# Optimization experiments

Hardware: AMD Instinct MI355X
Metric: run time of the kernel (lower is better)

Reference implementation:

```python
import jax, jax.numpy as jnp
import numpy as np

SQ, B, NH, HD = 2048, 2, 16, 128  # seq, batch, heads, head_dim


def setup_inputs() -> dict:
    key = jax.random.key(0)
    kq, kk, kv = jax.random.split(key, 3)
    shape = (SQ, B, NH, HD)
    return {
        "query": jax.random.normal(kq, shape, dtype=jnp.float32),
        "key": jax.random.normal(kk, shape, dtype=jnp.float32),
        "value": jax.random.normal(kv, shape, dtype=jnp.float32),
        "attention_mask": jnp.ones((B, 1, SQ, SQ), dtype=bool),
    }


def reference(query, key, value, attention_mask):
    # query/key/value: [s, b, n, h]
    sq, b, n_heads, hn = query.shape
    norm_factor = jnp.sqrt(jnp.asarray(hn, query.dtype))
    # QK^T -> [b, n, sq, sk]
    scores = jnp.einsum("sbnh,tbnh->bnst", query, key) / norm_factor
    probs = jax.nn.softmax(scores, axis=-1, where=attention_mask)
    # PV -> [s, b, n, h]  (dropout is identity at p=0.0 / eval)
    context = jnp.einsum("bnst,tbnh->sbnh", probs, value)
    return context.reshape(sq, b, n_heads * hn)
```

## Files before the change

### kernel.cpp

```cpp
#include <hip/hip_runtime.h>
#include <hip/hip_bf16.h>
#include <math.h>


#define SQ 2048
#define NBH 32
#define HD 128
#define RSTRIDE 4096
#define BQ 256
#define BK 64
#define NKT (SQ / BK)
#define HELEMS (SQ * HD)
#define SCALE_LOG2E 0.12751879523499918f
#define THR_LOG2 8.0f

typedef __attribute__((ext_vector_type(4)))  float f32x4;
typedef __attribute__((ext_vector_type(16))) float f32x16;
typedef __attribute__((ext_vector_type(4)))  short s16x4;
typedef __attribute__((ext_vector_type(8)))  short s16x8;

#define MFMA32(a, b, c) __builtin_amdgcn_mfma_f32_32x32x16_bf16((a), (b), (c), 0, 0, 0)
#define WAITV(N) asm volatile("s_waitcnt vmcnt(" #N ")" ::: "memory")

__device__ __forceinline__ short f2bf(float f) {
    __hip_bfloat16 h = __float2bfloat16(f);
    return __builtin_bit_cast(short, h);
}
__device__ __forceinline__ unsigned pk2(float lo, float hi) {
    unsigned r;
    asm("v_cvt_pk_bf16_f32 %0, %1, %2" : "=v"(r) : "v"(lo), "v"(hi));
    return r;
}

__device__ __forceinline__ void stage16(const void* g, void* l) {
    __builtin_amdgcn_global_load_lds(
        (const __attribute__((address_space(1))) unsigned int*)g,
        (__attribute__((address_space(3))) unsigned int*)l, 16, 0, 0);
}

__global__ __launch_bounds__(256) void prep_qk(const float* __restrict__ Q,
                                               const float* __restrict__ K,
                                               short* __restrict__ wq,
                                               short* __restrict__ wk) {
    const int id = blockIdx.x * 256 + threadIdx.x;
    const int bh = id >> 15;
    const int s  = (id >> 4) & 2047;
    const int c  = id & 15;
    const size_t outoff = (size_t)bh * HELEMS + (size_t)s * HD + c * 8;
    {
        const float* src = Q + (size_t)s * RSTRIDE + bh * HD + c * 8;
        f32x4 a = *(const f32x4*)src;
        f32x4 b = *(const f32x4*)(src + 4);
        s16x8 f;
        #pragma unroll
        for (int j = 0; j < 4; ++j) {
            f[j]     = f2bf(a[j] * SCALE_LOG2E);
            f[4 + j] = f2bf(b[j] * SCALE_LOG2E);
        }
        *(s16x8*)(wq + outoff) = f;
    }
    {
        const int cl = c ^ (s & 7);
        const float* src = K + (size_t)s * RSTRIDE + bh * HD + cl * 8;
        f32x4 a = *(const f32x4*)src;
        f32x4 b = *(const f32x4*)(src + 4);
        s16x8 f;
        #pragma unroll
        for (int j = 0; j < 4; ++j) { f[j] = f2bf(a[j]); f[4 + j] = f2bf(b[j]); }
        *(s16x8*)(wk + outoff) = f;
    }
}

__global__ __launch_bounds__(256) void prep_v(const float* __restrict__ V,
                                              short* __restrict__ wv) {
    const int kt = blockIdx.x;
    const int bh = blockIdx.y;
    const int tid = threadIdx.x;
    __shared__ short L[64 * 132];

    #pragma unroll
    for (int it = 0; it < 8; ++it) {
        const int id = it * 256 + tid;
        const int row = id >> 5, p = id & 31;
        f32x4 a = *(const f32x4*)(V + (size_t)(kt * BK + row) * RSTRIDE + bh * HD + p * 4);
        s16x4 f;
        #pragma unroll
        for (int j = 0; j < 4; ++j) f[j] = f2bf(a[j]);
        *(s16x4*)&L[row * 132 + p * 4] = f;
    }
    __syncthreads();
    #pragma unroll
    for (int it = 0; it < 4; ++it) {
        const int id = it * 256 + tid;
        const int dim = id >> 3, c = id & 7;
        const int klb = (c ^ (dim & 7)) * 8;
        s16x8 f;
        #pragma unroll
        for (int j = 0; j < 8; ++j) f[j] = L[(klb + j) * 132 + dim];
        *(s16x8*)(wv + (size_t)bh * HELEMS + (size_t)dim * SQ + kt * BK + c * 8) = f;
    }
}

__global__ __launch_bounds__(512) void fa_fwd3(const short* __restrict__ Qb,
                                               const short* __restrict__ Kb,
                                               const short* __restrict__ Vb,
                                               float* __restrict__ O) {
    const int id  = blockIdx.x;
    const int xcd = id & 7;
    const int s8  = id >> 3;
    const int bh  = xcd * 4 + (s8 >> 3);
    const int qt  = s8 & 7;

    const int tid  = threadIdx.x;
    const int w    = tid >> 6;
    const int lane = tid & 63;
    const int l32  = lane & 31;
    const int hi   = lane >> 5;

    __shared__ short Kt[3][BK * HD];
    __shared__ short Vt[3][HD * BK];

    const size_t hb = (size_t)bh * HELEMS;
    const int q = qt * BQ + w * 32 + l32;

    s16x8 qf[8];
    {
        const short* qp = Qb + hb + (size_t)q * HD + hi * 8;
        #pragma unroll
        for (int kd = 0; kd < 8; ++kd) qf[kd] = *(const s16x8*)(qp + kd * 16);
    }

    f32x16 acc[4];
    #pragma unroll
    for (int db = 0; db < 4; ++db)
        #pragma unroll
        for (int i = 0; i < 16; ++i) acc[db][i] = 0.0f;
    float m = -INFINITY, l = 0.0f;

    auto STAGE = [&](int kt, int buf) {
        if (w < 4) {
            const short* kg = Kb + hb + (size_t)kt * (BK * HD) + w * 2048 + lane * 8;
            short* ld = &Kt[buf][w * 2048 + lane * 8];
            #pragma unroll
            for (int j = 0; j < 4; ++j)
                stage16(kg + j * 512, ld + j * 512);
        } else {
            const int w4 = w - 4;
            #pragma unroll
            for (int j = 0; j < 4; ++j) {
                const int dim = w4 * 32 + j * 8 + (lane >> 3);
                const short* vg = Vb + hb + (size_t)dim * SQ + kt * BK + (lane & 7) * 8;
                stage16(vg, &Vt[buf][(w4 * 32 + j * 8) * BK + lane * 8]);
            }
        }
    };

    STAGE(0, 0);
    STAGE(1, 1);
    int bc = 0;

    for (int kt = 0; kt < NKT; ++kt) {
        if (kt + 1 < NKT) { WAITV(4); } else { WAITV(0); }
        __builtin_amdgcn_s_barrier();
        if (kt + 2 < NKT) {
            const int bs = bc + 2 >= 3 ? bc - 1 : bc + 2;
            STAGE(kt + 2, bs);
        }

        f32x16 sc[2];
        __builtin_amdgcn_s_setprio(1);
        #pragma unroll
        for (int kb = 0; kb < 2; ++kb) {
            #pragma unroll
            for (int i = 0; i < 16; ++i) sc[kb][i] = 0.0f;
            const int key = kb * 32 + l32;
            #pragma unroll
            for (int kd = 0; kd < 8; ++kd) {
                const int elem = key * HD + (((kd << 1) | hi) ^ (key & 7)) * 8;
                s16x8 kf = *(const s16x8*)&Kt[bc][elem];
                sc[kb] = MFMA32(kf, qf[kd], sc[kb]);
            }
        }
        __builtin_amdgcn_s_setprio(0);

        float mt0 = sc[0][0], mt1 = sc[0][1], mt2 = sc[0][2], mt3 = sc[0][3];
        #pragma unroll
        for (int kb = 0; kb < 2; ++kb)
            #pragma unroll
            for (int r = 0; r < 16; r += 4) {
                if (kb == 0 && r == 0) continue;
                mt0 = fmaxf(mt0, sc[kb][r + 0]);
                mt1 = fmaxf(mt1, sc[kb][r + 1]);
                mt2 = fmaxf(mt2, sc[kb][r + 2]);
                mt3 = fmaxf(mt3, sc[kb][r + 3]);
            }
        const float mt = fmaxf(fmaxf(mt0, mt1), fmaxf(mt2, mt3));
        const float m0 = fmaxf(mt, __shfl_xor(mt, 32, 64));
        const bool need = (m0 > m + THR_LOG2);
        const float mn = need ? fmaxf(m, m0) : m;
        if (__any(need)) {
            const float alpha = exp2f(m - mn);
            m = mn;
            l *= alpha;
            #pragma unroll
            for (int db = 0; db < 4; ++db) acc[db] *= alpha;
        }
        float lsp0 = 0.f, lsp1 = 0.f, lsp2 = 0.f, lsp3 = 0.f;
        #pragma unroll
        for (int kb = 0; kb < 2; ++kb)
            #pragma unroll
            for (int r = 0; r < 16; r += 4) {
                float p0 = exp2f(sc[kb][r + 0] - m);
                float p1 = exp2f(sc[kb][r + 1] - m);
                float p2 = exp2f(sc[kb][r + 2] - m);
                float p3 = exp2f(sc[kb][r + 3] - m);
                sc[kb][r + 0] = p0; sc[kb][r + 1] = p1;
                sc[kb][r + 2] = p2; sc[kb][r + 3] = p3;
                lsp0 += p0; lsp1 += p1; lsp2 += p2; lsp3 += p3;
            }
        l += (lsp0 + lsp1) + (lsp2 + lsp3);

        s16x8 pa[4];
        #pragma unroll
        for (int ks = 0; ks < 4; ++ks) {
            const int kb = ks >> 1;
            const int j  = (2 * ks) & 3, j2 = (2 * ks + 1) & 3;
            unsigned a0 = pk2(sc[kb][4 * j + 0],  sc[kb][4 * j + 1]);
            unsigned a1 = pk2(sc[kb][4 * j + 2],  sc[kb][4 * j + 3]);
            unsigned b0 = pk2(sc[kb][4 * j2 + 0], sc[kb][4 * j2 + 1]);
            unsigned b1 = pk2(sc[kb][4 * j2 + 2], sc[kb][4 * j2 + 3]);
#if __has_builtin(__builtin_amdgcn_permlane32_swap)
            auto r0 = __builtin_amdgcn_permlane32_swap(a0, b0, false, false);
            auto r1 = __builtin_amdgcn_permlane32_swap(a1, b1, false, false);
            union { unsigned u[4]; s16x8 v; } P;
            P.u[0] = r0[0]; P.u[1] = r1[0]; P.u[2] = r0[1]; P.u[3] = r1[1];
#else
            const unsigned s0 = __shfl_xor(hi ? a0 : b0, 32, 64);
            const unsigned s1 = __shfl_xor(hi ? a1 : b1, 32, 64);
            union { unsigned u[4]; s16x8 v; } P;
            P.u[0] = hi ? s0 : a0; P.u[1] = hi ? s1 : a1;
            P.u[2] = hi ? b0 : s0; P.u[3] = hi ? b1 : s1;
#endif
            pa[ks] = P.v;
        }

        __builtin_amdgcn_s_setprio(1);
        #pragma unroll
        for (int db = 0; db < 4; ++db) {
            const int dim = db * 32 + l32;
            #pragma unroll
            for (int ks = 0; ks < 4; ++ks) {
                const int elem = dim * BK + ((((ks << 1) | hi) ^ (dim & 7)) << 3);
                s16x8 vf = *(const s16x8*)&Vt[bc][elem];
                acc[db] = MFMA32(vf, pa[ks], acc[db]);
            }
        }
        __builtin_amdgcn_s_setprio(0);

        bc = bc + 1 >= 3 ? 0 : bc + 1;
    }

    const float lf = l + __shfl_xor(l, 32, 64);
    const float invl = 1.0f / lf;
    float* op = O + (size_t)q * RSTRIDE + bh * HD;
    #pragma unroll
    for (int db = 0; db < 4; ++db)
        #pragma unroll
        for (int j = 0; j < 4; ++j) {
            f32x4 o;
            #pragma unroll
            for (int r = 0; r < 4; ++r) o[r] = acc[db][4 * j + r] * invl;
            *(f32x4*)(op + db * 32 + j * 8 + hi * 4) = o;
        }
}

__global__ __launch_bounds__(256) void fa_fwd_legacy(const float* __restrict__ Q,
                                                     const float* __restrict__ K,
                                                     const float* __restrict__ V,
                                                     float* __restrict__ O) {
    const int qt   = blockIdx.x;
    const int bh   = blockIdx.y;
    const int tid  = threadIdx.x;
    const int w    = tid >> 6;
    const int lane = tid & 63;
    const int l16  = lane & 15;
    const int lg   = lane >> 4;

    __shared__ short Kt[BK * HD];
    __shared__ short Vt[HD * BK];
    __shared__ short Pl[4][16 * 72];

    const int headoff = bh * HD;
    s16x8 qf[4];
    {
        const int qrow = qt * 64 + w * 16 + l16;
        const float* qp = Q + (size_t)qrow * RSTRIDE + headoff + lg * 8;
        #pragma unroll
        for (int ks = 0; ks < 4; ++ks) {
            f32x4 a = *(const f32x4*)(qp + ks * 32);
            f32x4 b = *(const f32x4*)(qp + ks * 32 + 4);
            s16x8 f;
            #pragma unroll
            for (int j = 0; j < 4; ++j) {
                f[j]     = f2bf(a[j] * SCALE_LOG2E);
                f[4 + j] = f2bf(b[j] * SCALE_LOG2E);
            }
            qf[ks] = f;
        }
    }
    f32x4 acc[8];
    #pragma unroll
    for (int i = 0; i < 8; ++i)
        #pragma unroll
        for (int j = 0; j < 4; ++j) acc[i][j] = 0.0f;
    float mrow[4], lrow[4];
    #pragma unroll
    for (int r = 0; r < 4; ++r) { mrow[r] = -INFINITY; lrow[r] = 0.0f; }
    const int skey = tid >> 2;
    const int sdc  = tid & 3;
    const int va   = tid >> 3;
    const int vdc  = tid & 7;

    for (int kt = 0; kt < NKT; ++kt) {
        __syncthreads();
        {
            const float* kp = K + (size_t)(kt * BK + skey) * RSTRIDE + headoff;
            #pragma unroll
            for (int c = 0; c < 4; ++c) {
                const int d0 = c * 32 + sdc * 8;
                f32x4 a = *(const f32x4*)(kp + d0);
                f32x4 b = *(const f32x4*)(kp + d0 + 4);
                s16x8 f;
                #pragma unroll
                for (int j = 0; j < 4; ++j) { f[j] = f2bf(a[j]); f[4 + j] = f2bf(b[j]); }
                const int elem = (skey * HD + d0) ^ ((skey & 7) << 3);
                *(s16x8*)&Kt[elem] = f;
            }
        }
        {
            const float* vp0 = V + (size_t)(kt * BK + va * 2) * RSTRIDE + headoff;
            const float* vp1 = vp0 + RSTRIDE;
            #pragma unroll
            for (int c = 0; c < 4; ++c) {
                const int d0 = c * 32 + vdc * 4;
                f32x4 a0 = *(const f32x4*)(vp0 + d0);
                f32x4 a1 = *(const f32x4*)(vp1 + d0);
                #pragma unroll
                for (int j = 0; j < 4; ++j) {
                    const int dim = d0 + j;
                    const int s = (dim ^ (dim >> 3)) & 7;
                    const int elem = (dim * BK + va * 2) ^ (s << 3);
                    union { short u[2]; int i; } pr;
                    pr.u[0] = f2bf(a0[j]);
                    pr.u[1] = f2bf(a1[j]);
                    *(int*)&Vt[elem] = pr.i;
                }
            }
        }
        __syncthreads();
        f32x4 sc[4];
        #pragma unroll
        for (int t = 0; t < 4; ++t) {
            #pragma unroll
            for (int j = 0; j < 4; ++j) sc[t][j] = 0.0f;
            const int key = t * 16 + l16;
            #pragma unroll
            for (int ks = 0; ks < 4; ++ks) {
                const int elem = (key * HD + ks * 32 + lg * 8) ^ ((key & 7) << 3);
                s16x8 kf = *(const s16x8*)&Kt[elem];
                sc[t] = __builtin_amdgcn_mfma_f32_16x16x32_bf16(qf[ks], kf, sc[t], 0, 0, 0);
            }
        }
        float alpha[4];
        #pragma unroll
        for (int r = 0; r < 4; ++r) {
            float m0 = fmaxf(fmaxf(sc[0][r], sc[1][r]), fmaxf(sc[2][r], sc[3][r]));
            #pragma unroll
            for (int d = 1; d < 16; d <<= 1) m0 = fmaxf(m0, __shfl_xor(m0, d, 64));
            const float mnew = fmaxf(mrow[r], m0);
            alpha[r] = exp2f(mrow[r] - mnew);
            mrow[r] = mnew;
        }
        float rsum[4] = {0.f, 0.f, 0.f, 0.f};
        #pragma unroll
        for (int t = 0; t < 4; ++t)
            #pragma unroll
            for (int r = 0; r < 4; ++r) {
                const float p = exp2f(sc[t][r] - mrow[r]);
                sc[t][r] = p;
                rsum[r] += p;
            }
        #pragma unroll
        for (int r = 0; r < 4; ++r) {
            #pragma unroll
            for (int d = 1; d < 16; d <<= 1) rsum[r] += __shfl_xor(rsum[r], d, 64);
            lrow[r] = lrow[r] * alpha[r] + rsum[r];
        }
        #pragma unroll
        for (int ct = 0; ct < 8; ++ct)
            #pragma unroll
            for (int r = 0; r < 4; ++r) acc[ct][r] *= alpha[r];
        #pragma unroll
        for (int t = 0; t < 4; ++t)
            #pragma unroll
            for (int r = 0; r < 4; ++r)
                Pl[w][(lg * 4 + r) * 72 + t * 16 + l16] = f2bf(sc[t][r]);
        s16x8 pf[2];
        #pragma unroll
        for (int ks = 0; ks < 2; ++ks)
            pf[ks] = *(const s16x8*)&Pl[w][l16 * 72 + ks * 32 + lg * 8];
        #pragma unroll
        for (int ct = 0; ct < 8; ++ct) {
            const int dim = ct * 16 + l16;
            const int s = (dim ^ (dim >> 3)) & 7;
            #pragma unroll
            for (int ks = 0; ks < 2; ++ks) {
                const int elem = (dim * BK + ks * 32 + lg * 8) ^ (s << 3);
                s16x8 vf = *(const s16x8*)&Vt[elem];
                acc[ct] = __builtin_amdgcn_mfma_f32_16x16x32_bf16(pf[ks], vf, acc[ct], 0, 0, 0);
            }
        }
    }
    float inv_l[4];
    #pragma unroll
    for (int r = 0; r < 4; ++r) inv_l[r] = 1.0f / lrow[r];
    const int orow0 = qt * 64 + w * 16;
    #pragma unroll
    for (int ct = 0; ct < 8; ++ct) {
        const int col = ct * 16 + l16;
        #pragma unroll
        for (int r = 0; r < 4; ++r) {
            const int row = orow0 + lg * 4 + r;
            O[(size_t)row * RSTRIDE + headoff + col] = acc[ct][r] * inv_l[r];
        }
    }
}

extern "C" void kernel_launch(void* const* d_in, const int* in_sizes, int n_in,
                              void* d_out, int out_size, void* d_ws, size_t ws_size,
                              hipStream_t stream) {
    const float* Q = (const float*)d_in[0];
    const float* K = (const float*)d_in[1];
    const float* V = (const float*)d_in[2];
    float* O = (float*)d_out;

    const size_t need = (size_t)3 * NBH * HELEMS * sizeof(short);
    if (ws_size >= need) {
        short* wq = (short*)d_ws;
        short* wk = wq + (size_t)NBH * HELEMS;
        short* wv = wk + (size_t)NBH * HELEMS;
        prep_qk<<<4096, 256, 0, stream>>>(Q, K, wq, wk);
        prep_v<<<dim3(NKT, NBH), 256, 0, stream>>>(V, wv);
        fa_fwd3<<<(SQ / BQ) * NBH, 512, 0, stream>>>(wq, wk, wv, O);
    } else {
        fa_fwd_legacy<<<dim3(SQ / 64, NBH), 256, 0, stream>>>(Q, K, V, O);
    }
}
```

Measured before the change: 133.2 us.

## Software-pipeline QK^T of next tile with softmax and PV of current tile

Splits the attention loop body into QK^T, softmax/pack and PV stages and unrolls by two with two score/probability register sets. The QK^T MFMAs for tile t+1 are issued between the softmax of tile t and its PV product, so matrix work can overlap the exponent and max math. The explicit vmcnt waits are replaced by full __syncthreads barriers, two per pair of tiles. This adds register pressure from the duplicated score buffers, which may cause spills at 512 threads. The barriers may also wait on outstanding prefetches sooner than before.

Result: faster. 119.2 us (-10.5%).

```diff
diff --git a/kernel.cpp b/kernel.cpp
--- a/kernel.cpp
+++ b/kernel.cpp
@@ -20,7 +20,6 @@
 typedef __attribute__((ext_vector_type(8)))  short s16x8;
 
 #define MFMA32(a, b, c) __builtin_amdgcn_mfma_f32_32x32x16_bf16((a), (b), (c), 0, 0, 0)
-#define WAITV(N) asm volatile("s_waitcnt vmcnt(" #N ")" ::: "memory")
 
 __device__ __forceinline__ short f2bf(float f) {
     __hip_bfloat16 h = __float2bfloat16(f);
@@ -101,7 +100,7 @@
     }
 }
 
-__global__ __launch_bounds__(512) void fa_fwd3(const short* __restrict__ Qb,
+__global__ __launch_bounds__(512) void fa_fwd4(const short* __restrict__ Qb,
                                                const short* __restrict__ Kb,
                                                const short* __restrict__ Vb,
                                                float* __restrict__ O) {
@@ -155,19 +154,8 @@
         }
     };
 
-    STAGE(0, 0);
-    STAGE(1, 1);
-    int bc = 0;
-
-    for (int kt = 0; kt < NKT; ++kt) {
-        if (kt + 1 < NKT) { WAITV(4); } else { WAITV(0); }
-        __builtin_amdgcn_s_barrier();
-        if (kt + 2 < NKT) {
-            const int bs = bc + 2 >= 3 ? bc - 1 : bc + 2;
-            STAGE(kt + 2, bs);
-        }
-
-        f32x16 sc[2];
+    auto QKT = [&](int bufi, f32x16* sc) {
+        const short* Kb_ = Kt[bufi];
         __builtin_amdgcn_s_setprio(1);
         #pragma unroll
         for (int kb = 0; kb < 2; ++kb) {
@@ -177,12 +165,14 @@
             #pragma unroll
             for (int kd = 0; kd < 8; ++kd) {
                 const int elem = key * HD + (((kd << 1) | hi) ^ (key & 7)) * 8;
-                s16x8 kf = *(const s16x8*)&Kt[bc][elem];
+                s16x8 kf = *(const s16x8*)&Kb_[elem];
                 sc[kb] = MFMA32(kf, qf[kd], sc[kb]);
             }
         }
         __builtin_amdgcn_s_setprio(0);
-
+    };
+
+    auto SOFTPACK = [&](f32x16* sc, s16x8* pa) {
         float mt0 = sc[0][0], mt1 = sc[0][1], mt2 = sc[0][2], mt3 = sc[0][3];
         #pragma unroll
         for (int kb = 0; kb < 2; ++kb)
@@ -220,7 +210,6 @@
             }
         l += (lsp0 + lsp1) + (lsp2 + lsp3);
 
-        s16x8 pa[4];
         #pragma unroll
         for (int ks = 0; ks < 4; ++ks) {
             const int kb = ks >> 1;
@@ -243,7 +232,10 @@
 #endif
             pa[ks] = P.v;
         }
-
+    };
+
+    auto PV = [&](int bufi, s16x8* pa) {
+        const short* Vb_ = Vt[bufi];
         __builtin_amdgcn_s_setprio(1);
         #pragma unroll
         for (int db = 0; db < 4; ++db) {
@@ -251,13 +243,34 @@
             #pragma unroll
             for (int ks = 0; ks < 4; ++ks) {
                 const int elem = dim * BK + ((((ks << 1) | hi) ^ (dim & 7)) << 3);
-                s16x8 vf = *(const s16x8*)&Vt[bc][elem];
+                s16x8 vf = *(const s16x8*)&Vb_[elem];
                 acc[db] = MFMA32(vf, pa[ks], acc[db]);
             }
         }
         __builtin_amdgcn_s_setprio(0);
-
-        bc = bc + 1 >= 3 ? 0 : bc + 1;
+    };
+
+    f32x16 scA[2], scB[2];
+    s16x8 paA[4], paB[4];
+
+    STAGE(0, 0);
+    __syncthreads();
+    QKT(0, scA);
+    STAGE(1, 1);
+
+    #pragma unroll 1
+    for (int i = 0; i < NKT / 2; ++i) {
+        const int t0 = 2 * i;
+        __syncthreads();
+        if (t0 + 2 < NKT) STAGE(t0 + 2, (t0 + 2) % 3);
+        SOFTPACK(scA, paA);
+        if (t0 + 1 < NKT) QKT((t0 + 1) % 3, scB);
+        PV(t0 % 3, paA);
+        __syncthreads();
+        if (t0 + 3 < NKT) STAGE(t0 + 3, (t0 + 3) % 3);
+        SOFTPACK(scB, paB);
+        if (t0 + 2 < NKT) QKT((t0 + 2) % 3, scA);
+        PV((t0 + 1) % 3, paB);
     }
 
     const float lf = l + __shfl_xor(l, 32, 64);
@@ -451,7 +464,7 @@
         short* wv = wk + (size_t)NBH * HELEMS;
         prep_qk<<<4096, 256, 0, stream>>>(Q, K, wq, wk);
         prep_v<<<dim3(NKT, NBH), 256, 0, stream>>>(V, wv);
-        fa_fwd3<<<(SQ / BQ) * NBH, 512, 0, stream>>>(wq, wk, wv, O);
+        fa_fwd4<<<(SQ / BQ) * NBH, 512, 0, stream>>>(wq, wk, wv, O);
     } else {
         fa_fwd_legacy<<<dim3(SQ / 64, NBH), 256, 0, stream>>>(Q, K, V, O);
     }
```
